# Kernel optimization log

Measured on AMD Instinct MI355X. Metric: run time of the kernel, lower is better.

## Reference

```python
import jax, jax.numpy as jnp
import numpy as np

B = 8; R = 32; BS = 4; C = 128; H = 4; MLP = 512
SHIFT = BS // 2
N = BS ** 3            # tokens per window = 64
G = R // BS            # windows per axis = 8
NW = G ** 3            # windows per sample = 512
HD = C // H


def _rel_pos_index():
    # Faithful to the torch code: only coord 0 is scaled by (3*BS-1),
    # coords 1 and 2 are just added (index collisions are intentional here).
    coords = np.stack(np.meshgrid(np.arange(BS), np.arange(BS), np.arange(BS), indexing='ij'))
    cf = coords.reshape(3, -1)
    rel = (cf[:, :, None] - cf[:, None, :]).transpose(1, 2, 0).astype(np.int64)
    rel += BS - 1
    rel[:, :, 0] *= 3 * BS - 1
    return rel.sum(-1)  # (N, N)


def _attn_mask():
    img = np.zeros((R, R, R), np.float32)
    slices = (slice(0, -BS), slice(-BS, -SHIFT), slice(-SHIFT, None))
    cnt = 0
    for sx in slices:
        for sy in slices:
            for sz in slices:
                img[sx, sy, sz] = cnt
                cnt += 1
    boxes = img.reshape(G, BS, G, BS, G, BS).transpose(0, 2, 4, 1, 3, 5).reshape(-1, N)
    d = boxes[:, None, :] - boxes[:, :, None]  # (NW, N, N)
    return np.where(d != 0, np.float32(-100.0), np.float32(0.0))


_RPI = _rel_pos_index()
_MASK = _attn_mask()


def setup_inputs() -> dict:
    key = jax.random.key(0)
    ks = jax.random.split(key, 16)
    s = 0.02
    return {
        'inputs': jax.random.normal(ks[0], (B, R ** 3, C), jnp.float32),
        'qkv_w': jax.random.normal(ks[1], (C, 3 * C), jnp.float32) * s,
        'proj_w': jax.random.normal(ks[2], (C, C), jnp.float32) * s,
        'proj_b': jnp.zeros((C,), jnp.float32),
        'bias_table': jax.random.normal(ks[3], ((3 * BS - 1) ** 2, H), jnp.float32) * s,
        'g1': jnp.ones((C,), jnp.float32),
        'b1': jnp.zeros((C,), jnp.float32),
        'g2': jnp.ones((C,), jnp.float32),
        'b2': jnp.zeros((C,), jnp.float32),
        'w1': jax.random.normal(ks[4], (C, MLP), jnp.float32) * s,
        'bb1': jnp.zeros((MLP,), jnp.float32),
        'w2': jax.random.normal(ks[5], (MLP, C), jnp.float32) * s,
        'bb2': jnp.zeros((C,), jnp.float32),
    }


def _ln(x, g, b):
    m = x.mean(-1, keepdims=True)
    v = x.var(-1, keepdims=True)
    return (x - m) * jax.lax.rsqrt(v + 1e-5) * g + b


def reference(inputs, qkv_w, proj_w, proj_b, bias_table, g1, b1, g2, b2, w1, bb1, w2, bb2):
    rpi = jnp.asarray(_RPI)
    mask = jnp.asarray(_MASK)

    x = _ln(inputs, g1, b1).reshape(B, R, R, R, C)
    x = jnp.roll(x, (-SHIFT, -SHIFT, -SHIFT), axis=(1, 2, 3))
    # box partition -> (B*NW, N, C)
    boxes = x.reshape(B, G, BS, G, BS, G, BS, C).transpose(0, 1, 3, 5, 2, 4, 6, 7).reshape(-1, N, C)

    qkv = (boxes @ qkv_w).reshape(-1, N, 3, H, HD).transpose(2, 0, 3, 1, 4)
    q, k, v = qkv[0] * (HD ** -0.5), qkv[1], qkv[2]
    attn = jnp.einsum('bhnd,bhmd->bhnm', q, k)

    bias = bias_table[rpi.reshape(-1)].reshape(N, N, H).transpose(2, 0, 1)  # (H, N, N)
    attn = attn + bias[None]
    attn = attn.reshape(B, NW, H, N, N) + mask[None, :, None]
    attn = jax.nn.softmax(attn.reshape(-1, H, N, N), axis=-1)

    out = jnp.einsum('bhnm,bhmd->bhnd', attn, v).transpose(0, 2, 1, 3).reshape(-1, N, C)
    out = out @ proj_w + proj_b

    # box reverse + unshift
    out = out.reshape(B, G, G, G, BS, BS, BS, C).transpose(0, 1, 4, 2, 5, 3, 6, 7).reshape(B, R, R, R, C)
    out = jnp.roll(out, (SHIFT, SHIFT, SHIFT), axis=(1, 2, 3)).reshape(B, R ** 3, C)

    x = out * 0.5 + inputs
    h = _ln(x, g2, b2)
    h = jax.nn.gelu(h @ w1 + bb1, approximate=False) @ w2 + bb2
    return h * 0.5 + x
```

## Files before the change

### kernel.cpp

```cpp
#include <hip/hip_runtime.h>
#include <hip/hip_bf16.h>

typedef unsigned short u16;
typedef unsigned int u32;
typedef __attribute__((ext_vector_type(8))) short short8;
typedef __attribute__((ext_vector_type(4))) float f32x4;

__device__ __forceinline__ u16 f2bf(float x) {
  __hip_bfloat16 h = __float2bfloat16(x);
  return *reinterpret_cast<u16*>(&h);
}

__global__ __launch_bounds__(256) void k_wprep4(const float* __restrict__ qkv_w,
                                                const float* __restrict__ proj_w,
                                                const float* __restrict__ w1,
                                                const float* __restrict__ w2,
                                                u16* __restrict__ qkvT, u16* __restrict__ projT,
                                                u16* __restrict__ w1T, u16* __restrict__ w2T) {
  __shared__ float tile[64][65];
  const int b = blockIdx.x, t = threadIdx.x;
  const float* src; u16* dst; int K, N, tk, tn;
  if (b < 12)      { src = qkv_w;  dst = qkvT;  K = 128; N = 384; tk = b / 6;        tn = b % 6; }
  else if (b < 16) { src = proj_w; dst = projT; K = 128; N = 128; tk = (b - 12) / 2; tn = (b - 12) % 2; }
  else if (b < 32) { src = w1;     dst = w1T;   K = 128; N = 512; tk = (b - 16) / 8; tn = (b - 16) % 8; }
  else             { src = w2;     dst = w2T;   K = 512; N = 128; tk = (b - 32) / 2; tn = (b - 32) % 2; }
  const int rb = t >> 6, c = t & 63;
  #pragma unroll
  for (int i = 0; i < 16; ++i) {
    int r = i * 4 + rb;
    tile[r][c] = src[(size_t)(tk * 64 + r) * N + tn * 64 + c];
  }
  __syncthreads();
  #pragma unroll
  for (int i = 0; i < 16; ++i) {
    int rr = i * 4 + rb;
    dst[(size_t)(tn * 64 + rr) * K + tk * 64 + c] = f2bf(tile[c][rr]);
  }
}

__global__ __launch_bounds__(256, 2) void k_all(const float* __restrict__ inputs,
                                                const u16* __restrict__ qkvT,
                                                const u16* __restrict__ projT,
                                                const float* __restrict__ proj_b,
                                                const float* __restrict__ btab,
                                                const float* __restrict__ g1,
                                                const float* __restrict__ b1,
                                                const u16* __restrict__ w1T,
                                                const u16* __restrict__ w2T,
                                                const float* __restrict__ g2,
                                                const float* __restrict__ b2,
                                                const float* __restrict__ bb1,
                                                const float* __restrict__ bb2,
                                                float* __restrict__ out) {
  __shared__ __align__(16) char lds[76800];
  u16* A_s  = (u16*)lds;
  u16* Q_s  = (u16*)(lds + 19456);
  u16* K_s  = (u16*)(lds + 36864);
  u16* P_s  = (u16*)lds;
  u16* O_s  = (u16*)(lds + 36864);
  u16* Vt_s = (u16*)(lds + 54272);
  float* bias_s = (float*)(lds + 72704);
  float* red    = (float*)(lds + 74752);
  float* X_s = (float*)lds;
  u16* A2_s  = (u16*)(lds + 36864);
  u16* H0    = (u16*)(lds + 54272);
  u16* H1    = (u16*)(lds + 63488);

  const int t = threadIdx.x, wv = t >> 6, lane = t & 63;
  const int m = lane & 15, q4 = lane >> 4;
  const int bw = blockIdx.x;
  const int wbox = bw & 511, bsm = bw >> 9;
  const int gx = wbox >> 6, gy = (wbox >> 3) & 7, gz = wbox & 7;

  for (int i = t; i < 484; i += 256) bias_s[(i & 3) * 128 + (i >> 2)] = btab[i];

  short8 bq[4][2];
  #pragma unroll
  for (int kc = 0; kc < 4; ++kc)
    #pragma unroll
    for (int nt2 = 0; nt2 < 2; ++nt2)
      bq[kc][nt2] = *(const short8*)(qkvT + (size_t)(wv * 32 + nt2 * 16 + m) * 128 + kc * 32 + q4 * 8);

  {
    const int r1 = t >> 2, seg = t & 3;
    const int ix = r1 >> 4, iy = (r1 >> 2) & 3, iz = r1 & 3;
    const int X = (gx * 4 + ix + 2) & 31, Y = (gy * 4 + iy + 2) & 31, Z = (gz * 4 + iz + 2) & 31;
    const size_t orig = ((size_t)bsm << 15) + (size_t)(X * 1024 + Y * 32 + Z);
    const float4* x4 = (const float4*)(inputs + orig * 128 + seg * 32);
    float vals[32];
    float s = 0.f, ss = 0.f;
    #pragma unroll
    for (int i = 0; i < 8; ++i) {
      float4 v = x4[i];
      vals[4 * i] = v.x; vals[4 * i + 1] = v.y; vals[4 * i + 2] = v.z; vals[4 * i + 3] = v.w;
      s += v.x + v.y + v.z + v.w;
      ss += v.x * v.x + v.y * v.y + v.z * v.z + v.w * v.w;
    }
    red[r1 * 8 + seg] = s; red[r1 * 8 + 4 + seg] = ss;
    float sum = red[r1 * 8 + 0] + red[r1 * 8 + 1] + red[r1 * 8 + 2] + red[r1 * 8 + 3];
    float sq  = red[r1 * 8 + 4] + red[r1 * 8 + 5] + red[r1 * 8 + 6] + red[r1 * 8 + 7];
    float mean = sum * 0.0078125f;
    float var = sq * 0.0078125f - mean * mean;
    float rs = rsqrtf(var + 1e-5f);
    #pragma unroll
    for (int i = 0; i < 32; ++i) {
      int c = seg * 32 + i;
      A_s[r1 * 152 + c] = f2bf((vals[i] - mean) * rs * g1[c] + b1[c]);
    }
  }
  __syncthreads();

  short8 bk[4][2];
  #pragma unroll
  for (int kc = 0; kc < 4; ++kc)
    #pragma unroll
    for (int nt2 = 0; nt2 < 2; ++nt2)
      bk[kc][nt2] = *(const short8*)(qkvT + (size_t)(128 + wv * 32 + nt2 * 16 + m) * 128 + kc * 32 + q4 * 8);

  short8 af[4][4];
  #pragma unroll
  for (int kc = 0; kc < 4; ++kc)
    #pragma unroll
    for (int mt = 0; mt < 4; ++mt)
      af[kc][mt] = *(const short8*)(A_s + (mt * 16 + m) * 152 + kc * 32 + q4 * 8);

  f32x4 zero = {0.f, 0.f, 0.f, 0.f};

  {
    f32x4 acc1[4][2];
    #pragma unroll
    for (int mt = 0; mt < 4; ++mt)
      #pragma unroll
      for (int nt2 = 0; nt2 < 2; ++nt2) acc1[mt][nt2] = zero;
    #pragma unroll
    for (int kc = 0; kc < 4; ++kc)
      #pragma unroll
      for (int mt = 0; mt < 4; ++mt)
        #pragma unroll
        for (int nt2 = 0; nt2 < 2; ++nt2)
          acc1[mt][nt2] = __builtin_amdgcn_mfma_f32_16x16x32_bf16(af[kc][mt], bq[kc][nt2], acc1[mt][nt2], 0, 0, 0);
    #pragma unroll
    for (int mt = 0; mt < 4; ++mt)
      #pragma unroll
      for (int nt2 = 0; nt2 < 2; ++nt2)
        #pragma unroll
        for (int r = 0; r < 4; ++r)
          Q_s[(mt * 16 + q4 * 4 + r) * 136 + wv * 32 + nt2 * 16 + m] =
              f2bf(acc1[mt][nt2][r] * 0.17677669529663687f);
  }

  short8 bv[4][2];
  #pragma unroll
  for (int kc = 0; kc < 4; ++kc)
    #pragma unroll
    for (int nt2 = 0; nt2 < 2; ++nt2)
      bv[kc][nt2] = *(const short8*)(qkvT + (size_t)(256 + wv * 32 + nt2 * 16 + m) * 128 + kc * 32 + q4 * 8);

  {
    f32x4 acc1[4][2];
    #pragma unroll
    for (int mt = 0; mt < 4; ++mt)
      #pragma unroll
      for (int nt2 = 0; nt2 < 2; ++nt2) acc1[mt][nt2] = zero;
    #pragma unroll
    for (int kc = 0; kc < 4; ++kc)
      #pragma unroll
      for (int mt = 0; mt < 4; ++mt)
        #pragma unroll
        for (int nt2 = 0; nt2 < 2; ++nt2)
          acc1[mt][nt2] = __builtin_amdgcn_mfma_f32_16x16x32_bf16(af[kc][mt], bk[kc][nt2], acc1[mt][nt2], 0, 0, 0);
    #pragma unroll
    for (int mt = 0; mt < 4; ++mt)
      #pragma unroll
      for (int nt2 = 0; nt2 < 2; ++nt2)
        #pragma unroll
        for (int r = 0; r < 4; ++r)
          K_s[(mt * 16 + q4 * 4 + r) * 136 + wv * 32 + nt2 * 16 + m] = f2bf(acc1[mt][nt2][r]);
  }

  {
    f32x4 acc1[4][2];
    #pragma unroll
    for (int mt = 0; mt < 4; ++mt)
      #pragma unroll
      for (int nt2 = 0; nt2 < 2; ++nt2) acc1[mt][nt2] = zero;
    #pragma unroll
    for (int kc = 0; kc < 4; ++kc)
      #pragma unroll
      for (int mt = 0; mt < 4; ++mt)
        #pragma unroll
        for (int nt2 = 0; nt2 < 2; ++nt2)
          acc1[mt][nt2] = __builtin_amdgcn_mfma_f32_16x16x32_bf16(af[kc][mt], bv[kc][nt2], acc1[mt][nt2], 0, 0, 0);
    #pragma unroll
    for (int mt = 0; mt < 4; ++mt)
      #pragma unroll
      for (int nt2 = 0; nt2 < 2; ++nt2)
        #pragma unroll
        for (int r = 0; r < 4; ++r)
          Vt_s[wv * 2304 + (nt2 * 16 + m) * 72 + mt * 16 + q4 * 4 + r] = f2bf(acc1[mt][nt2][r]);
  }

  short8 qf[4], kf[4];
  #pragma unroll
  for (int ti = 0; ti < 4; ++ti) {
    qf[ti] = *(const short8*)(Q_s + (ti * 16 + m) * 136 + wv * 32 + q4 * 8);
    kf[ti] = *(const short8*)(K_s + (ti * 16 + m) * 136 + wv * 32 + q4 * 8);
  }
  __syncthreads();

  f32x4 S[4][4];
  #pragma unroll
  for (int ti = 0; ti < 4; ++ti)
    #pragma unroll
    for (int tj = 0; tj < 4; ++tj) S[ti][tj] = zero;
  #pragma unroll
  for (int ti = 0; ti < 4; ++ti)
    #pragma unroll
    for (int tj = 0; tj < 4; ++tj)
      S[ti][tj] = __builtin_amdgcn_mfma_f32_16x16x32_bf16(qf[ti], kf[tj], S[ti][tj], 0, 0, 0);

  int catx[4], caty[4], catz[4];
  #pragma unroll
  for (int a = 0; a < 4; ++a) {
    catx[a] = (gx < 7) ? 0 : ((a < 2) ? 1 : 2);
    caty[a] = (gy < 7) ? 0 : ((a < 2) ? 1 : 2);
    catz[a] = (gz < 7) ? 0 : ((a < 2) ? 1 : 2);
  }
  const int cy = (m >> 2) & 3, cz = m & 3;
  int labc[4], labr[16];
  #pragma unroll
  for (int tj = 0; tj < 4; ++tj) labc[tj] = catx[tj] * 9 + caty[cy] * 3 + catz[cz];
  #pragma unroll
  for (int ti = 0; ti < 4; ++ti)
    #pragma unroll
    for (int r = 0; r < 4; ++r) labr[ti * 4 + r] = catx[ti] * 9 + caty[q4] * 3 + catz[r];

  #pragma unroll
  for (int ti = 0; ti < 4; ++ti)
    #pragma unroll
    for (int tj = 0; tj < 4; ++tj) {
      int K0 = 11 * (ti - tj + 3) + (q4 + 3 - cy) + (3 - cz);
      #pragma unroll
      for (int r = 0; r < 4; ++r) {
        float v = S[ti][tj][r] + bias_s[wv * 128 + K0 + r];
        if (labr[ti * 4 + r] != labc[tj]) v -= 100.f;
        S[ti][tj][r] = v;
      }
    }

  float mx[16], sm[16];
  #pragma unroll
  for (int ti = 0; ti < 4; ++ti)
    #pragma unroll
    for (int r = 0; r < 4; ++r)
      mx[ti * 4 + r] = fmaxf(fmaxf(S[ti][0][r], S[ti][1][r]), fmaxf(S[ti][2][r], S[ti][3][r]));
  #pragma unroll
  for (int off = 1; off < 16; off <<= 1)
    #pragma unroll
    for (int i = 0; i < 16; ++i) mx[i] = fmaxf(mx[i], __shfl_xor(mx[i], off, 64));
  #pragma unroll
  for (int ti = 0; ti < 4; ++ti)
    #pragma unroll
    for (int r = 0; r < 4; ++r) {
      float e0 = __expf(S[ti][0][r] - mx[ti * 4 + r]);
      float e1 = __expf(S[ti][1][r] - mx[ti * 4 + r]);
      float e2 = __expf(S[ti][2][r] - mx[ti * 4 + r]);
      float e3 = __expf(S[ti][3][r] - mx[ti * 4 + r]);
      S[ti][0][r] = e0; S[ti][1][r] = e1; S[ti][2][r] = e2; S[ti][3][r] = e3;
      sm[ti * 4 + r] = (e0 + e1) + (e2 + e3);
    }
  #pragma unroll
  for (int off = 1; off < 16; off <<= 1)
    #pragma unroll
    for (int i = 0; i < 16; ++i) sm[i] += __shfl_xor(sm[i], off, 64);
  #pragma unroll
  for (int i = 0; i < 16; ++i) sm[i] = 1.f / sm[i];

  #pragma unroll
  for (int ti = 0; ti < 4; ++ti)
    #pragma unroll
    for (int tj = 0; tj < 4; ++tj)
      #pragma unroll
      for (int r = 0; r < 4; ++r)
        P_s[wv * 4608 + (ti * 16 + q4 * 4 + r) * 72 + tj * 16 + m] = f2bf(S[ti][tj][r]);

  f32x4 O[4][2];
  #pragma unroll
  for (int ti = 0; ti < 4; ++ti)
    #pragma unroll
    for (int tv = 0; tv < 2; ++tv) O[ti][tv] = zero;
  #pragma unroll
  for (int ks = 0; ks < 2; ++ks) {
    short8 pa[4], vb[2];
    #pragma unroll
    for (int ti = 0; ti < 4; ++ti)
      pa[ti] = *(const short8*)(P_s + wv * 4608 + (ti * 16 + m) * 72 + ks * 32 + q4 * 8);
    #pragma unroll
    for (int tv = 0; tv < 2; ++tv)
      vb[tv] = *(const short8*)(Vt_s + wv * 2304 + (tv * 16 + m) * 72 + ks * 32 + q4 * 8);
    #pragma unroll
    for (int ti = 0; ti < 4; ++ti)
      #pragma unroll
      for (int tv = 0; tv < 2; ++tv)
        O[ti][tv] = __builtin_amdgcn_mfma_f32_16x16x32_bf16(pa[ti], vb[tv], O[ti][tv], 0, 0, 0);
  }

  #pragma unroll
  for (int ti = 0; ti < 4; ++ti)
    #pragma unroll
    for (int tv = 0; tv < 2; ++tv)
      #pragma unroll
      for (int r = 0; r < 4; ++r)
        O_s[(ti * 16 + q4 * 4 + r) * 136 + wv * 32 + tv * 16 + m] = f2bf(O[ti][tv][r] * sm[ti * 4 + r]);

  short8 bp[4][2];
  #pragma unroll
  for (int kc = 0; kc < 4; ++kc)
    #pragma unroll
    for (int nt2 = 0; nt2 < 2; ++nt2)
      bp[kc][nt2] = *(const short8*)(projT + (size_t)(wv * 32 + nt2 * 16 + m) * 128 + kc * 32 + q4 * 8);
  float pb[2] = {proj_b[wv * 32 + m], proj_b[wv * 32 + 16 + m]};

  __syncthreads();

  short8 af2[4][4];
  #pragma unroll
  for (int kc = 0; kc < 4; ++kc)
    #pragma unroll
    for (int mt = 0; mt < 4; ++mt)
      af2[kc][mt] = *(const short8*)(O_s + (mt * 16 + m) * 136 + kc * 32 + q4 * 8);
  f32x4 acc2[4][2];
  #pragma unroll
  for (int mt = 0; mt < 4; ++mt)
    #pragma unroll
    for (int nt2 = 0; nt2 < 2; ++nt2) acc2[mt][nt2] = zero;
  #pragma unroll
  for (int kc = 0; kc < 4; ++kc)
    #pragma unroll
    for (int mt = 0; mt < 4; ++mt)
      #pragma unroll
      for (int nt2 = 0; nt2 < 2; ++nt2)
        acc2[mt][nt2] = __builtin_amdgcn_mfma_f32_16x16x32_bf16(af2[kc][mt], bp[kc][nt2], acc2[mt][nt2], 0, 0, 0);

  #pragma unroll
  for (int mt = 0; mt < 4; ++mt)
    #pragma unroll
    for (int nt2 = 0; nt2 < 2; ++nt2)
      #pragma unroll
      for (int r = 0; r < 4; ++r)
        X_s[(mt * 16 + q4 * 4 + r) * 132 + wv * 32 + nt2 * 16 + m] = 0.5f * (acc2[mt][nt2][r] + pb[nt2]);

  __syncthreads();

  const u16* w1base = w1T + (size_t)(wv * 16 + m) * 128 + q4 * 8;
  short8 b1p0[4], b1p1[4];
  #pragma unroll
  for (int kc = 0; kc < 4; ++kc) b1p0[kc] = *(const short8*)(w1base + kc * 32);
  #pragma unroll
  for (int kc = 0; kc < 4; ++kc) b1p1[kc] = *(const short8*)(w1base + (size_t)64 * 128 + kc * 32);
  float bias1[8];
  #pragma unroll
  for (int nt = 0; nt < 8; ++nt) bias1[nt] = bb1[nt * 64 + wv * 16 + m];

  {
    const int r1 = t >> 2, seg = t & 3;
    const int ix = r1 >> 4, iy = (r1 >> 2) & 3, iz = r1 & 3;
    const int X = (gx * 4 + ix + 2) & 31, Y = (gy * 4 + iy + 2) & 31, Z = (gz * 4 + iz + 2) & 31;
    const size_t orig = ((size_t)bsm << 15) + (size_t)(X * 1024 + Y * 32 + Z);
    const float4* x4 = (const float4*)(inputs + orig * 128 + seg * 32);
    float vals[32];
    float s = 0.f, ss = 0.f;
    #pragma unroll
    for (int i = 0; i < 8; ++i) {
      float4 v = x4[i];
      float* xp = X_s + r1 * 132 + seg * 32 + 4 * i;
      float a0 = xp[0] + v.x, a1 = xp[1] + v.y, a2 = xp[2] + v.z, a3 = xp[3] + v.w;
      xp[0] = a0; xp[1] = a1; xp[2] = a2; xp[3] = a3;
      vals[4 * i] = a0; vals[4 * i + 1] = a1; vals[4 * i + 2] = a2; vals[4 * i + 3] = a3;
      s += a0 + a1 + a2 + a3;
      ss += a0 * a0 + a1 * a1 + a2 * a2 + a3 * a3;
    }
    red[r1 * 8 + seg] = s; red[r1 * 8 + 4 + seg] = ss;
    float sum = red[r1 * 8 + 0] + red[r1 * 8 + 1] + red[r1 * 8 + 2] + red[r1 * 8 + 3];
    float sq  = red[r1 * 8 + 4] + red[r1 * 8 + 5] + red[r1 * 8 + 6] + red[r1 * 8 + 7];
    float mean = sum * 0.0078125f;
    float var = sq * 0.0078125f - mean * mean;
    float rs = rsqrtf(var + 1e-5f);
    #pragma unroll
    for (int i = 0; i < 32; ++i) {
      int c = seg * 32 + i;
      A2_s[r1 * 136 + c] = f2bf((vals[i] - mean) * rs * g2[c] + b2[c]);
    }
  }
  __syncthreads();

  short8 am[4][4];
  #pragma unroll
  for (int kc = 0; kc < 4; ++kc)
    #pragma unroll
    for (int mt = 0; mt < 4; ++mt)
      am[kc][mt] = *(const short8*)(A2_s + (mt * 16 + m) * 136 + kc * 32 + q4 * 8);

  f32x4 acc[4][2];
  #pragma unroll
  for (int mt = 0; mt < 4; ++mt)
    #pragma unroll
    for (int nt2 = 0; nt2 < 2; ++nt2) acc[mt][nt2] = zero;

  #pragma unroll
  for (int nt = 0; nt < 8; ++nt) {
    u16* Hb = (nt & 1) ? H1 : H0;
    f32x4 hacc[4];
    #pragma unroll
    for (int mt = 0; mt < 4; ++mt) hacc[mt] = zero;
    if (nt & 1) {
      #pragma unroll
      for (int kc = 0; kc < 4; ++kc)
        #pragma unroll
        for (int mt = 0; mt < 4; ++mt)
          hacc[mt] = __builtin_amdgcn_mfma_f32_16x16x32_bf16(am[kc][mt], b1p1[kc], hacc[mt], 0, 0, 0);
    } else {
      #pragma unroll
      for (int kc = 0; kc < 4; ++kc)
        #pragma unroll
        for (int mt = 0; mt < 4; ++mt)
          hacc[mt] = __builtin_amdgcn_mfma_f32_16x16x32_bf16(am[kc][mt], b1p0[kc], hacc[mt], 0, 0, 0);
    }

    short8 b2f[2][2];
    #pragma unroll
    for (int kc2 = 0; kc2 < 2; ++kc2)
      #pragma unroll
      for (int nt2 = 0; nt2 < 2; ++nt2)
        b2f[kc2][nt2] = *(const short8*)(w2T + (size_t)(wv * 32 + nt2 * 16 + m) * 512 +
                                         nt * 64 + kc2 * 32 + q4 * 8);

    float bias = bias1[nt];
    #pragma unroll
    for (int mt = 0; mt < 4; ++mt)
      #pragma unroll
      for (int r = 0; r < 4; ++r) {
        float v = hacc[mt][r] + bias;
        float v2 = v * v;
        float qe = v * __builtin_fmaf(-0.07135482f, v2, -1.5957691f);
        float te = __expf(qe);
        float gl = v * __builtin_amdgcn_rcpf(1.f + te);
        Hb[(mt * 16 + q4 * 4 + r) * 72 + wv * 16 + m] = f2bf(gl);
      }
    __syncthreads();

    if (nt < 6) {
      const u16* p = w1base + (size_t)(nt + 2) * 64 * 128;
      if (nt & 1) {
        #pragma unroll
        for (int kc = 0; kc < 4; ++kc) b1p1[kc] = *(const short8*)(p + kc * 32);
      } else {
        #pragma unroll
        for (int kc = 0; kc < 4; ++kc) b1p0[kc] = *(const short8*)(p + kc * 32);
      }
    }

    #pragma unroll
    for (int kc2 = 0; kc2 < 2; ++kc2) {
      short8 a2[4];
      #pragma unroll
      for (int mt = 0; mt < 4; ++mt)
        a2[mt] = *(const short8*)(Hb + (mt * 16 + m) * 72 + kc2 * 32 + q4 * 8);
      #pragma unroll
      for (int mt = 0; mt < 4; ++mt)
        #pragma unroll
        for (int nt2 = 0; nt2 < 2; ++nt2)
          acc[mt][nt2] = __builtin_amdgcn_mfma_f32_16x16x32_bf16(a2[mt], b2f[kc2][nt2],
                                                                 acc[mt][nt2], 0, 0, 0);
    }
  }

  float ob[2] = {bb2[wv * 32 + m], bb2[wv * 32 + 16 + m]};
  #pragma unroll
  for (int mt = 0; mt < 4; ++mt)
    #pragma unroll
    for (int r = 0; r < 4; ++r) {
      int nn = mt * 16 + q4 * 4 + r;
      int ix = nn >> 4, iy = (nn >> 2) & 3, iz = nn & 3;
      int X = (gx * 4 + ix + 2) & 31, Y = (gy * 4 + iy + 2) & 31, Z = (gz * 4 + iz + 2) & 31;
      size_t orig = ((size_t)bsm << 15) + (size_t)(X * 1024 + Y * 32 + Z);
      #pragma unroll
      for (int nt2 = 0; nt2 < 2; ++nt2) {
        int col = wv * 32 + nt2 * 16 + m;
        float v = acc[mt][nt2][r] + ob[nt2];
        out[orig * 128 + col] = 0.5f * v + X_s[nn * 132 + col];
      }
    }
}

extern "C" void kernel_launch(void* const* d_in, const int* in_sizes, int n_in,
                              void* d_out, int out_size, void* d_ws, size_t ws_size,
                              hipStream_t stream) {
  const float* inputs = (const float*)d_in[0];
  const float* qkv_w  = (const float*)d_in[1];
  const float* proj_w = (const float*)d_in[2];
  const float* proj_b = (const float*)d_in[3];
  const float* btab   = (const float*)d_in[4];
  const float* g1     = (const float*)d_in[5];
  const float* b1     = (const float*)d_in[6];
  const float* g2     = (const float*)d_in[7];
  const float* b2     = (const float*)d_in[8];
  const float* w1     = (const float*)d_in[9];
  const float* bb1    = (const float*)d_in[10];
  const float* w2     = (const float*)d_in[11];
  const float* bb2    = (const float*)d_in[12];
  float* out = (float*)d_out;

  char* ws = (char*)d_ws;
  u16* qkvT  = (u16*)(ws + 0);
  u16* projT = (u16*)(ws + 98304);
  u16* w1T   = (u16*)(ws + 131072);
  u16* w2T   = (u16*)(ws + 262144);

  k_wprep4<<<48, 256, 0, stream>>>(qkv_w, proj_w, w1, w2, qkvT, projT, w1T, w2T);
  k_all<<<4096, 256, 0, stream>>>(inputs, qkvT, projT, proj_b, btab, g1, b1,
                                  w1T, w2T, g2, b2, bb1, bb2, out);
}
```

Measured before the change: 481.7 us.

## Transpose MFMA operand roles, precompute bias fragments, shrink LDS for higher occupancy

Swaps the A/B operand order in several MFMAs so accumulator rows map to tokens. This allows packed 8-byte bf16 stores to LDS and vectorised f32x4 output writes instead of scalar scatter. The relative-position bias is precomputed per lane into a global fragment buffer by an extra prep block. LayerNorm reductions now use warp shuffles instead of LDS, and the residual is kept in registers. Together these cut LDS from 75KB to 52KB and raise launch bounds to 3 blocks per CU, which risks register pressure and spills.

```diff
diff --git a/kernel.cpp b/kernel.cpp
--- a/kernel.cpp
+++ b/kernel.cpp
@@ -4,21 +4,44 @@
 typedef unsigned short u16;
 typedef unsigned int u32;
 typedef __attribute__((ext_vector_type(8))) short short8;
+typedef __attribute__((ext_vector_type(2))) unsigned int u32x2;
 typedef __attribute__((ext_vector_type(4))) float f32x4;
 
 __device__ __forceinline__ u16 f2bf(float x) {
   __hip_bfloat16 h = __float2bfloat16(x);
   return *reinterpret_cast<u16*>(&h);
 }
+__device__ __forceinline__ u32 pk2(float a, float b) {
+  return (u32)f2bf(a) | ((u32)f2bf(b) << 16);
+}
+__device__ __forceinline__ float bflo(u32 u) { return __uint_as_float(u << 16); }
+__device__ __forceinline__ float bfhi(u32 u) { return __uint_as_float(u & 0xffff0000u); }
 
 __global__ __launch_bounds__(256) void k_wprep4(const float* __restrict__ qkv_w,
                                                 const float* __restrict__ proj_w,
                                                 const float* __restrict__ w1,
                                                 const float* __restrict__ w2,
+                                                const float* __restrict__ btab,
                                                 u16* __restrict__ qkvT, u16* __restrict__ projT,
-                                                u16* __restrict__ w1T, u16* __restrict__ w2T) {
+                                                u16* __restrict__ w1T, u16* __restrict__ w2T,
+                                                u32* __restrict__ bfrag) {
+  const int b = blockIdx.x, t = threadIdx.x;
+  if (b == 48) {
+    const int h = t >> 6, m = t & 15, q4 = (t >> 4) & 3;
+    const int my = m >> 2, mz = m & 3;
+    for (int g = 0; g < 16; ++g) {
+      int ti = g >> 2, tj = g & 3;
+      int base = 11 * (tj - ti + 3) + (my - q4 + 3) + (mz + 3);
+      float v0 = btab[(base - 0) * 4 + h];
+      float v1 = btab[(base - 1) * 4 + h];
+      float v2 = btab[(base - 2) * 4 + h];
+      float v3 = btab[(base - 3) * 4 + h];
+      bfrag[(g * 256 + t) * 2 + 0] = pk2(v0, v1);
+      bfrag[(g * 256 + t) * 2 + 1] = pk2(v2, v3);
+    }
+    return;
+  }
   __shared__ float tile[64][65];
-  const int b = blockIdx.x, t = threadIdx.x;
   const float* src; u16* dst; int K, N, tk, tn;
   if (b < 12)      { src = qkv_w;  dst = qkvT;  K = 128; N = 384; tk = b / 6;        tn = b % 6; }
   else if (b < 16) { src = proj_w; dst = projT; K = 128; N = 128; tk = (b - 12) / 2; tn = (b - 12) % 2; }
@@ -38,11 +61,11 @@
   }
 }
 
-__global__ __launch_bounds__(256, 2) void k_all(const float* __restrict__ inputs,
+__global__ __launch_bounds__(256, 3) void k_all(const float* __restrict__ inputs,
                                                 const u16* __restrict__ qkvT,
                                                 const u16* __restrict__ projT,
                                                 const float* __restrict__ proj_b,
-                                                const float* __restrict__ btab,
+                                                const u32* __restrict__ bfrag,
                                                 const float* __restrict__ g1,
                                                 const float* __restrict__ b1,
                                                 const u16* __restrict__ w1T,
@@ -52,34 +75,13 @@
                                                 const float* __restrict__ bb1,
                                                 const float* __restrict__ bb2,
                                                 float* __restrict__ out) {
-  __shared__ __align__(16) char lds[76800];
-  u16* A_s  = (u16*)lds;
-  u16* Q_s  = (u16*)(lds + 19456);
-  u16* K_s  = (u16*)(lds + 36864);
-  u16* P_s  = (u16*)lds;
-  u16* O_s  = (u16*)(lds + 36864);
-  u16* Vt_s = (u16*)(lds + 54272);
-  float* bias_s = (float*)(lds + 72704);
-  float* red    = (float*)(lds + 74752);
-  float* X_s = (float*)lds;
-  u16* A2_s  = (u16*)(lds + 36864);
-  u16* H0    = (u16*)(lds + 54272);
-  u16* H1    = (u16*)(lds + 63488);
+  __shared__ __align__(16) char lds[53248];
 
   const int t = threadIdx.x, wv = t >> 6, lane = t & 63;
   const int m = lane & 15, q4 = lane >> 4;
   const int bw = blockIdx.x;
   const int wbox = bw & 511, bsm = bw >> 9;
   const int gx = wbox >> 6, gy = (wbox >> 3) & 7, gz = wbox & 7;
-
-  for (int i = t; i < 484; i += 256) bias_s[(i & 3) * 128 + (i >> 2)] = btab[i];
-
-  short8 bq[4][2];
-  #pragma unroll
-  for (int kc = 0; kc < 4; ++kc)
-    #pragma unroll
-    for (int nt2 = 0; nt2 < 2; ++nt2)
-      bq[kc][nt2] = *(const short8*)(qkvT + (size_t)(wv * 32 + nt2 * 16 + m) * 128 + kc * 32 + q4 * 8);
 
   {
     const int r1 = t >> 2, seg = t & 3;
@@ -96,116 +98,132 @@
       s += v.x + v.y + v.z + v.w;
       ss += v.x * v.x + v.y * v.y + v.z * v.z + v.w * v.w;
     }
-    red[r1 * 8 + seg] = s; red[r1 * 8 + 4 + seg] = ss;
-    float sum = red[r1 * 8 + 0] + red[r1 * 8 + 1] + red[r1 * 8 + 2] + red[r1 * 8 + 3];
-    float sq  = red[r1 * 8 + 4] + red[r1 * 8 + 5] + red[r1 * 8 + 6] + red[r1 * 8 + 7];
-    float mean = sum * 0.0078125f;
-    float var = sq * 0.0078125f - mean * mean;
+    s += __shfl_xor(s, 1, 64);  s += __shfl_xor(s, 2, 64);
+    ss += __shfl_xor(ss, 1, 64); ss += __shfl_xor(ss, 2, 64);
+    float mean = s * 0.0078125f;
+    float var = ss * 0.0078125f - mean * mean;
     float rs = rsqrtf(var + 1e-5f);
     #pragma unroll
-    for (int i = 0; i < 32; ++i) {
-      int c = seg * 32 + i;
-      A_s[r1 * 152 + c] = f2bf((vals[i] - mean) * rs * g1[c] + b1[c]);
-    }
-  }
-  __syncthreads();
-
-  short8 bk[4][2];
+    for (int v8 = 0; v8 < 4; ++v8) {
+      short8 w;
+      #pragma unroll
+      for (int j = 0; j < 8; ++j) {
+        int c = seg * 32 + v8 * 8 + j;
+        w[j] = (short)f2bf((vals[v8 * 8 + j] - mean) * rs * g1[c] + b1[c]);
+      }
+      *(short8*)(lds + r1 * 272 + seg * 64 + v8 * 16) = w;
+    }
+  }
+  __syncthreads();
+
+  short8 af[4][4];
   #pragma unroll
   for (int kc = 0; kc < 4; ++kc)
     #pragma unroll
-    for (int nt2 = 0; nt2 < 2; ++nt2)
-      bk[kc][nt2] = *(const short8*)(qkvT + (size_t)(128 + wv * 32 + nt2 * 16 + m) * 128 + kc * 32 + q4 * 8);
-
-  short8 af[4][4];
-  #pragma unroll
-  for (int kc = 0; kc < 4; ++kc)
+    for (int jt = 0; jt < 4; ++jt)
+      af[kc][jt] = *(const short8*)(lds + (jt * 16 + m) * 272 + kc * 64 + q4 * 16);
+  __syncthreads();
+
+  f32x4 zero = {0.f, 0.f, 0.f, 0.f};
+
+  {
+    short8 wq[4][2];
+    #pragma unroll
+    for (int kc = 0; kc < 4; ++kc)
+      #pragma unroll
+      for (int it = 0; it < 2; ++it)
+        wq[kc][it] = *(const short8*)(qkvT + (size_t)(wv * 32 + it * 16 + m) * 128 + kc * 32 + q4 * 8);
+    f32x4 acc[2][4];
+    #pragma unroll
+    for (int it = 0; it < 2; ++it)
+      #pragma unroll
+      for (int jt = 0; jt < 4; ++jt) acc[it][jt] = zero;
+    #pragma unroll
+    for (int kc = 0; kc < 4; ++kc)
+      #pragma unroll
+      for (int it = 0; it < 2; ++it)
+        #pragma unroll
+        for (int jt = 0; jt < 4; ++jt)
+          acc[it][jt] = __builtin_amdgcn_mfma_f32_16x16x32_bf16(wq[kc][it], af[kc][jt], acc[it][jt], 0, 0, 0);
+    #pragma unroll
+    for (int it = 0; it < 2; ++it)
+      #pragma unroll
+      for (int jt = 0; jt < 4; ++jt) {
+        f32x4 a = acc[it][jt];
+        u32x2 w = {pk2(a[0] * 0.17677669529663687f, a[1] * 0.17677669529663687f),
+                   pk2(a[2] * 0.17677669529663687f, a[3] * 0.17677669529663687f)};
+        *(u32x2*)(lds + (jt * 16 + m) * 272 + (wv * 32 + it * 16 + q4 * 4) * 2) = w;
+      }
+  }
+
+  {
+    short8 wk[4][2];
+    #pragma unroll
+    for (int kc = 0; kc < 4; ++kc)
+      #pragma unroll
+      for (int it = 0; it < 2; ++it)
+        wk[kc][it] = *(const short8*)(qkvT + (size_t)(128 + wv * 32 + it * 16 + m) * 128 + kc * 32 + q4 * 8);
+    f32x4 acc[2][4];
+    #pragma unroll
+    for (int it = 0; it < 2; ++it)
+      #pragma unroll
+      for (int jt = 0; jt < 4; ++jt) acc[it][jt] = zero;
+    #pragma unroll
+    for (int kc = 0; kc < 4; ++kc)
+      #pragma unroll
+      for (int it = 0; it < 2; ++it)
+        #pragma unroll
+        for (int jt = 0; jt < 4; ++jt)
+          acc[it][jt] = __builtin_amdgcn_mfma_f32_16x16x32_bf16(wk[kc][it], af[kc][jt], acc[it][jt], 0, 0, 0);
+    #pragma unroll
+    for (int it = 0; it < 2; ++it)
+      #pragma unroll
+      for (int jt = 0; jt < 4; ++jt) {
+        f32x4 a = acc[it][jt];
+        u32x2 w = {pk2(a[0], a[1]), pk2(a[2], a[3])};
+        *(u32x2*)(lds + 17408 + (jt * 16 + m) * 272 + (wv * 32 + it * 16 + q4 * 4) * 2) = w;
+      }
+  }
+
+  {
+    short8 wvv[4][2];
+    #pragma unroll
+    for (int kc = 0; kc < 4; ++kc)
+      #pragma unroll
+      for (int n2 = 0; n2 < 2; ++n2)
+        wvv[kc][n2] = *(const short8*)(qkvT + (size_t)(256 + wv * 32 + n2 * 16 + m) * 128 + kc * 32 + q4 * 8);
+    f32x4 acc[4][2];
     #pragma unroll
     for (int mt = 0; mt < 4; ++mt)
-      af[kc][mt] = *(const short8*)(A_s + (mt * 16 + m) * 152 + kc * 32 + q4 * 8);
-
-  f32x4 zero = {0.f, 0.f, 0.f, 0.f};
-
-  {
-    f32x4 acc1[4][2];
+      #pragma unroll
+      for (int n2 = 0; n2 < 2; ++n2) acc[mt][n2] = zero;
+    #pragma unroll
+    for (int kc = 0; kc < 4; ++kc)
+      #pragma unroll
+      for (int mt = 0; mt < 4; ++mt)
+        #pragma unroll
+        for (int n2 = 0; n2 < 2; ++n2)
+          acc[mt][n2] = __builtin_amdgcn_mfma_f32_16x16x32_bf16(af[kc][mt], wvv[kc][n2], acc[mt][n2], 0, 0, 0);
     #pragma unroll
     for (int mt = 0; mt < 4; ++mt)
       #pragma unroll
-      for (int nt2 = 0; nt2 < 2; ++nt2) acc1[mt][nt2] = zero;
-    #pragma unroll
-    for (int kc = 0; kc < 4; ++kc)
-      #pragma unroll
-      for (int mt = 0; mt < 4; ++mt)
-        #pragma unroll
-        for (int nt2 = 0; nt2 < 2; ++nt2)
-          acc1[mt][nt2] = __builtin_amdgcn_mfma_f32_16x16x32_bf16(af[kc][mt], bq[kc][nt2], acc1[mt][nt2], 0, 0, 0);
-    #pragma unroll
-    for (int mt = 0; mt < 4; ++mt)
-      #pragma unroll
-      for (int nt2 = 0; nt2 < 2; ++nt2)
-        #pragma unroll
-        for (int r = 0; r < 4; ++r)
-          Q_s[(mt * 16 + q4 * 4 + r) * 136 + wv * 32 + nt2 * 16 + m] =
-              f2bf(acc1[mt][nt2][r] * 0.17677669529663687f);
-  }
-
-  short8 bv[4][2];
-  #pragma unroll
-  for (int kc = 0; kc < 4; ++kc)
-    #pragma unroll
-    for (int nt2 = 0; nt2 < 2; ++nt2)
-      bv[kc][nt2] = *(const short8*)(qkvT + (size_t)(256 + wv * 32 + nt2 * 16 + m) * 128 + kc * 32 + q4 * 8);
-
-  {
-    f32x4 acc1[4][2];
-    #pragma unroll
-    for (int mt = 0; mt < 4; ++mt)
-      #pragma unroll
-      for (int nt2 = 0; nt2 < 2; ++nt2) acc1[mt][nt2] = zero;
-    #pragma unroll
-    for (int kc = 0; kc < 4; ++kc)
-      #pragma unroll
-      for (int mt = 0; mt < 4; ++mt)
-        #pragma unroll
-        for (int nt2 = 0; nt2 < 2; ++nt2)
-          acc1[mt][nt2] = __builtin_amdgcn_mfma_f32_16x16x32_bf16(af[kc][mt], bk[kc][nt2], acc1[mt][nt2], 0, 0, 0);
-    #pragma unroll
-    for (int mt = 0; mt < 4; ++mt)
-      #pragma unroll
-      for (int nt2 = 0; nt2 < 2; ++nt2)
-        #pragma unroll
-        for (int r = 0; r < 4; ++r)
-          K_s[(mt * 16 + q4 * 4 + r) * 136 + wv * 32 + nt2 * 16 + m] = f2bf(acc1[mt][nt2][r]);
-  }
-
-  {
-    f32x4 acc1[4][2];
-    #pragma unroll
-    for (int mt = 0; mt < 4; ++mt)
-      #pragma unroll
-      for (int nt2 = 0; nt2 < 2; ++nt2) acc1[mt][nt2] = zero;
-    #pragma unroll
-    for (int kc = 0; kc < 4; ++kc)
-      #pragma unroll
-      for (int mt = 0; mt < 4; ++mt)
-        #pragma unroll
-        for (int nt2 = 0; nt2 < 2; ++nt2)
-          acc1[mt][nt2] = __builtin_amdgcn_mfma_f32_16x16x32_bf16(af[kc][mt], bv[kc][nt2], acc1[mt][nt2], 0, 0, 0);
-    #pragma unroll
-    for (int mt = 0; mt < 4; ++mt)
-      #pragma unroll
-      for (int nt2 = 0; nt2 < 2; ++nt2)
-        #pragma unroll
-        for (int r = 0; r < 4; ++r)
-          Vt_s[wv * 2304 + (nt2 * 16 + m) * 72 + mt * 16 + q4 * 4 + r] = f2bf(acc1[mt][nt2][r]);
+      for (int n2 = 0; n2 < 2; ++n2) {
+        f32x4 a = acc[mt][n2];
+        u32x2 w = {pk2(a[0], a[1]), pk2(a[2], a[3])};
+        *(u32x2*)(lds + 34816 + wv * 4608 + (n2 * 16 + m) * 144 + mt * 32 + q4 * 8) = w;
+      }
   }
 
   short8 qf[4], kf[4];
   #pragma unroll
   for (int ti = 0; ti < 4; ++ti) {
-    qf[ti] = *(const short8*)(Q_s + (ti * 16 + m) * 136 + wv * 32 + q4 * 8);
-    kf[ti] = *(const short8*)(K_s + (ti * 16 + m) * 136 + wv * 32 + q4 * 8);
-  }
+    qf[ti] = *(const short8*)(lds + (ti * 16 + m) * 272 + wv * 64 + q4 * 16);
+    kf[ti] = *(const short8*)(lds + 17408 + (ti * 16 + m) * 272 + wv * 64 + q4 * 16);
+  }
+  u32x2 bu[16];
+  #pragma unroll
+  for (int g = 0; g < 16; ++g)
+    bu[g] = *(const u32x2*)(bfrag + (g * 256 + t) * 2);
   __syncthreads();
 
   f32x4 S[4][4];
@@ -217,7 +235,7 @@
   for (int ti = 0; ti < 4; ++ti)
     #pragma unroll
     for (int tj = 0; tj < 4; ++tj)
-      S[ti][tj] = __builtin_amdgcn_mfma_f32_16x16x32_bf16(qf[ti], kf[tj], S[ti][tj], 0, 0, 0);
+      S[ti][tj] = __builtin_amdgcn_mfma_f32_16x16x32_bf16(kf[ti], qf[tj], S[ti][tj], 0, 0, 0);
 
   int catx[4], caty[4], catz[4];
   #pragma unroll
@@ -227,130 +245,215 @@
     catz[a] = (gz < 7) ? 0 : ((a < 2) ? 1 : 2);
   }
   const int cy = (m >> 2) & 3, cz = m & 3;
-  int labc[4], labr[16];
-  #pragma unroll
-  for (int tj = 0; tj < 4; ++tj) labc[tj] = catx[tj] * 9 + caty[cy] * 3 + catz[cz];
+  int labq[4], labk[16];
+  #pragma unroll
+  for (int tj = 0; tj < 4; ++tj) labq[tj] = catx[tj] * 9 + caty[cy] * 3 + catz[cz];
   #pragma unroll
   for (int ti = 0; ti < 4; ++ti)
     #pragma unroll
-    for (int r = 0; r < 4; ++r) labr[ti * 4 + r] = catx[ti] * 9 + caty[q4] * 3 + catz[r];
+    for (int rr = 0; rr < 4; ++rr) labk[ti * 4 + rr] = catx[ti] * 9 + caty[q4] * 3 + catz[rr];
 
   #pragma unroll
   for (int ti = 0; ti < 4; ++ti)
     #pragma unroll
     for (int tj = 0; tj < 4; ++tj) {
-      int K0 = 11 * (ti - tj + 3) + (q4 + 3 - cy) + (3 - cz);
-      #pragma unroll
-      for (int r = 0; r < 4; ++r) {
-        float v = S[ti][tj][r] + bias_s[wv * 128 + K0 + r];
-        if (labr[ti * 4 + r] != labc[tj]) v -= 100.f;
-        S[ti][tj][r] = v;
-      }
-    }
-
-  float mx[16], sm[16];
+      u32x2 bp = bu[ti * 4 + tj];
+      #pragma unroll
+      for (int rr = 0; rr < 4; ++rr) {
+        float bv = (rr & 1) ? bfhi(bp[rr >> 1]) : bflo(bp[rr >> 1]);
+        float v = S[ti][tj][rr] + bv;
+        if (labk[ti * 4 + rr] != labq[tj]) v -= 100.f;
+        S[ti][tj][rr] = v;
+      }
+    }
+
+  float mx[4], sm[4];
+  #pragma unroll
+  for (int tj = 0; tj < 4; ++tj) {
+    float v = fmaxf(fmaxf(S[0][tj][0], S[0][tj][1]), fmaxf(S[0][tj][2], S[0][tj][3]));
+    #pragma unroll
+    for (int ti = 1; ti < 4; ++ti)
+      v = fmaxf(v, fmaxf(fmaxf(S[ti][tj][0], S[ti][tj][1]), fmaxf(S[ti][tj][2], S[ti][tj][3])));
+    v = fmaxf(v, __shfl_xor(v, 16, 64));
+    v = fmaxf(v, __shfl_xor(v, 32, 64));
+    mx[tj] = v;
+  }
+  #pragma unroll
+  for (int tj = 0; tj < 4; ++tj) {
+    float s = 0.f;
+    #pragma unroll
+    for (int ti = 0; ti < 4; ++ti)
+      #pragma unroll
+      for (int rr = 0; rr < 4; ++rr) {
+        float e = __expf(S[ti][tj][rr] - mx[tj]);
+        S[ti][tj][rr] = e;
+        s += e;
+      }
+    s += __shfl_xor(s, 16, 64);
+    s += __shfl_xor(s, 32, 64);
+    sm[tj] = 1.f / s;
+  }
+
   #pragma unroll
   for (int ti = 0; ti < 4; ++ti)
     #pragma unroll
-    for (int r = 0; r < 4; ++r)
-      mx[ti * 4 + r] = fmaxf(fmaxf(S[ti][0][r], S[ti][1][r]), fmaxf(S[ti][2][r], S[ti][3][r]));
-  #pragma unroll
-  for (int off = 1; off < 16; off <<= 1)
-    #pragma unroll
-    for (int i = 0; i < 16; ++i) mx[i] = fmaxf(mx[i], __shfl_xor(mx[i], off, 64));
-  #pragma unroll
-  for (int ti = 0; ti < 4; ++ti)
-    #pragma unroll
-    for (int r = 0; r < 4; ++r) {
-      float e0 = __expf(S[ti][0][r] - mx[ti * 4 + r]);
-      float e1 = __expf(S[ti][1][r] - mx[ti * 4 + r]);
-      float e2 = __expf(S[ti][2][r] - mx[ti * 4 + r]);
-      float e3 = __expf(S[ti][3][r] - mx[ti * 4 + r]);
-      S[ti][0][r] = e0; S[ti][1][r] = e1; S[ti][2][r] = e2; S[ti][3][r] = e3;
-      sm[ti * 4 + r] = (e0 + e1) + (e2 + e3);
-    }
-  #pragma unroll
-  for (int off = 1; off < 16; off <<= 1)
-    #pragma unroll
-    for (int i = 0; i < 16; ++i) sm[i] += __shfl_xor(sm[i], off, 64);
-  #pragma unroll
-  for (int i = 0; i < 16; ++i) sm[i] = 1.f / sm[i];
-
-  #pragma unroll
-  for (int ti = 0; ti < 4; ++ti)
-    #pragma unroll
-    for (int tj = 0; tj < 4; ++tj)
-      #pragma unroll
-      for (int r = 0; r < 4; ++r)
-        P_s[wv * 4608 + (ti * 16 + q4 * 4 + r) * 72 + tj * 16 + m] = f2bf(S[ti][tj][r]);
-
-  f32x4 O[4][2];
-  #pragma unroll
-  for (int ti = 0; ti < 4; ++ti)
-    #pragma unroll
-    for (int tv = 0; tv < 2; ++tv) O[ti][tv] = zero;
+    for (int tj = 0; tj < 4; ++tj) {
+      f32x4 a = S[ti][tj];
+      u32x2 w = {pk2(a[0], a[1]), pk2(a[2], a[3])};
+      *(u32x2*)(lds + wv * 8704 + (tj * 16 + m) * 136 + ti * 32 + q4 * 8) = w;
+    }
+
+  f32x4 accO[2][4];
+  #pragma unroll
+  for (int it = 0; it < 2; ++it)
+    #pragma unroll
+    for (int jt = 0; jt < 4; ++jt) accO[it][jt] = zero;
   #pragma unroll
   for (int ks = 0; ks < 2; ++ks) {
-    short8 pa[4], vb[2];
-    #pragma unroll
-    for (int ti = 0; ti < 4; ++ti)
-      pa[ti] = *(const short8*)(P_s + wv * 4608 + (ti * 16 + m) * 72 + ks * 32 + q4 * 8);
-    #pragma unroll
-    for (int tv = 0; tv < 2; ++tv)
-      vb[tv] = *(const short8*)(Vt_s + wv * 2304 + (tv * 16 + m) * 72 + ks * 32 + q4 * 8);
-    #pragma unroll
-    for (int ti = 0; ti < 4; ++ti)
-      #pragma unroll
-      for (int tv = 0; tv < 2; ++tv)
-        O[ti][tv] = __builtin_amdgcn_mfma_f32_16x16x32_bf16(pa[ti], vb[tv], O[ti][tv], 0, 0, 0);
-  }
-
-  #pragma unroll
-  for (int ti = 0; ti < 4; ++ti)
-    #pragma unroll
-    for (int tv = 0; tv < 2; ++tv)
-      #pragma unroll
-      for (int r = 0; r < 4; ++r)
-        O_s[(ti * 16 + q4 * 4 + r) * 136 + wv * 32 + tv * 16 + m] = f2bf(O[ti][tv][r] * sm[ti * 4 + r]);
-
-  short8 bp[4][2];
+    short8 vb[2], pa[4];
+    #pragma unroll
+    for (int it = 0; it < 2; ++it)
+      vb[it] = *(const short8*)(lds + 34816 + wv * 4608 + (it * 16 + m) * 144 + ks * 64 + q4 * 16);
+    #pragma unroll
+    for (int jt = 0; jt < 4; ++jt) {
+      u32x2 lo = *(const u32x2*)(lds + wv * 8704 + (jt * 16 + m) * 136 + ks * 64 + q4 * 16);
+      u32x2 hi = *(const u32x2*)(lds + wv * 8704 + (jt * 16 + m) * 136 + ks * 64 + q4 * 16 + 8);
+      union { u32 u[4]; short8 s; } c;
+      c.u[0] = lo[0]; c.u[1] = lo[1]; c.u[2] = hi[0]; c.u[3] = hi[1];
+      pa[jt] = c.s;
+    }
+    #pragma unroll
+    for (int it = 0; it < 2; ++it)
+      #pragma unroll
+      for (int jt = 0; jt < 4; ++jt)
+        accO[it][jt] = __builtin_amdgcn_mfma_f32_16x16x32_bf16(vb[it], pa[jt], accO[it][jt], 0, 0, 0);
+  }
+  __syncthreads();
+
+  #pragma unroll
+  for (int it = 0; it < 2; ++it)
+    #pragma unroll
+    for (int jt = 0; jt < 4; ++jt) {
+      f32x4 a = accO[it][jt];
+      float sc = sm[jt];
+      u32x2 w = {pk2(a[0] * sc, a[1] * sc), pk2(a[2] * sc, a[3] * sc)};
+      *(u32x2*)(lds + (jt * 16 + m) * 272 + (wv * 32 + it * 16 + q4 * 4) * 2) = w;
+    }
+  __syncthreads();
+
+  int origjt[4];
+  #pragma unroll
+  for (int jt = 0; jt < 4; ++jt) {
+    int X = (gx * 4 + jt + 2) & 31, Y = (gy * 4 + (m >> 2) + 2) & 31, Z = (gz * 4 + (m & 3) + 2) & 31;
+    origjt[jt] = (bsm << 15) + X * 1024 + Y * 32 + Z;
+  }
+  f32x4 xr[2][4];
+  {
+    short8 bp[4][2], of[4][4];
+    #pragma unroll
+    for (int kc = 0; kc < 4; ++kc)
+      #pragma unroll
+      for (int it = 0; it < 2; ++it)
+        bp[kc][it] = *(const short8*)(projT + (size_t)(wv * 32 + it * 16 + m) * 128 + kc * 32 + q4 * 8);
+    f32x4 inr[2][4];
+    #pragma unroll
+    for (int it = 0; it < 2; ++it)
+      #pragma unroll
+      for (int jt = 0; jt < 4; ++jt)
+        inr[it][jt] = *(const f32x4*)(inputs + (size_t)origjt[jt] * 128 + wv * 32 + it * 16 + q4 * 4);
+    f32x4 pbv[2];
+    #pragma unroll
+    for (int it = 0; it < 2; ++it)
+      pbv[it] = *(const f32x4*)(proj_b + wv * 32 + it * 16 + q4 * 4);
+    #pragma unroll
+    for (int kc = 0; kc < 4; ++kc)
+      #pragma unroll
+      for (int jt = 0; jt < 4; ++jt)
+        of[kc][jt] = *(const short8*)(lds + (jt * 16 + m) * 272 + kc * 64 + q4 * 16);
+    f32x4 acc[2][4];
+    #pragma unroll
+    for (int it = 0; it < 2; ++it)
+      #pragma unroll
+      for (int jt = 0; jt < 4; ++jt) acc[it][jt] = zero;
+    #pragma unroll
+    for (int kc = 0; kc < 4; ++kc)
+      #pragma unroll
+      for (int it = 0; it < 2; ++it)
+        #pragma unroll
+        for (int jt = 0; jt < 4; ++jt)
+          acc[it][jt] = __builtin_amdgcn_mfma_f32_16x16x32_bf16(bp[kc][it], of[kc][jt], acc[it][jt], 0, 0, 0);
+    #pragma unroll
+    for (int it = 0; it < 2; ++it)
+      #pragma unroll
+      for (int jt = 0; jt < 4; ++jt)
+        #pragma unroll
+        for (int rr = 0; rr < 4; ++rr)
+          xr[it][jt][rr] = 0.5f * (acc[it][jt][rr] + pbv[it][rr]) + inr[it][jt][rr];
+  }
+  __syncthreads();
+
+  float* red = (float*)(lds + 34816);
+  {
+    float sp[4], ssp[4];
+    #pragma unroll
+    for (int jt = 0; jt < 4; ++jt) {
+      float s = 0.f, ss2 = 0.f;
+      #pragma unroll
+      for (int it = 0; it < 2; ++it)
+        #pragma unroll
+        for (int rr = 0; rr < 4; ++rr) {
+          float v = xr[it][jt][rr];
+          s += v; ss2 += v * v;
+        }
+      s += __shfl_xor(s, 16, 64);  s += __shfl_xor(s, 32, 64);
+      ss2 += __shfl_xor(ss2, 16, 64); ss2 += __shfl_xor(ss2, 32, 64);
+      sp[jt] = s; ssp[jt] = ss2;
+    }
+    if (q4 == 0) {
+      #pragma unroll
+      for (int jt = 0; jt < 4; ++jt) {
+        red[(jt * 16 + m) * 8 + wv * 2 + 0] = sp[jt];
+        red[(jt * 16 + m) * 8 + wv * 2 + 1] = ssp[jt];
+      }
+    }
+  }
+  __syncthreads();
+
+  {
+    f32x4 g2v[2], b2v[2];
+    #pragma unroll
+    for (int it = 0; it < 2; ++it) {
+      g2v[it] = *(const f32x4*)(g2 + wv * 32 + it * 16 + q4 * 4);
+      b2v[it] = *(const f32x4*)(b2 + wv * 32 + it * 16 + q4 * 4);
+    }
+    #pragma unroll
+    for (int jt = 0; jt < 4; ++jt) {
+      f32x4 r0 = *(const f32x4*)(red + (jt * 16 + m) * 8);
+      f32x4 r1 = *(const f32x4*)(red + (jt * 16 + m) * 8 + 4);
+      float sum = r0[0] + r0[2] + r1[0] + r1[2];
+      float sq  = r0[1] + r0[3] + r1[1] + r1[3];
+      float mean = sum * 0.0078125f;
+      float var = sq * 0.0078125f - mean * mean;
+      float rs = rsqrtf(var + 1e-5f);
+      #pragma unroll
+      for (int it = 0; it < 2; ++it) {
+        float n0 = (xr[it][jt][0] - mean) * rs * g2v[it][0] + b2v[it][0];
+        float n1 = (xr[it][jt][1] - mean) * rs * g2v[it][1] + b2v[it][1];
+        float n2 = (xr[it][jt][2] - mean) * rs * g2v[it][2] + b2v[it][2];
+        float n3 = (xr[it][jt][3] - mean) * rs * g2v[it][3] + b2v[it][3];
+        u32x2 w = {pk2(n0, n1), pk2(n2, n3)};
+        *(u32x2*)(lds + 17408 + (jt * 16 + m) * 272 + (wv * 32 + it * 16 + q4 * 4) * 2) = w;
+      }
+    }
+  }
+  __syncthreads();
+
+  short8 am[4][4];
   #pragma unroll
   for (int kc = 0; kc < 4; ++kc)
     #pragma unroll
-    for (int nt2 = 0; nt2 < 2; ++nt2)
-      bp[kc][nt2] = *(const short8*)(projT + (size_t)(wv * 32 + nt2 * 16 + m) * 128 + kc * 32 + q4 * 8);
-  float pb[2] = {proj_b[wv * 32 + m], proj_b[wv * 32 + 16 + m]};
-
-  __syncthreads();
-
-  short8 af2[4][4];
-  #pragma unroll
-  for (int kc = 0; kc < 4; ++kc)
-    #pragma unroll
-    for (int mt = 0; mt < 4; ++mt)
-      af2[kc][mt] = *(const short8*)(O_s + (mt * 16 + m) * 136 + kc * 32 + q4 * 8);
-  f32x4 acc2[4][2];
-  #pragma unroll
-  for (int mt = 0; mt < 4; ++mt)
-    #pragma unroll
-    for (int nt2 = 0; nt2 < 2; ++nt2) acc2[mt][nt2] = zero;
-  #pragma unroll
-  for (int kc = 0; kc < 4; ++kc)
-    #pragma unroll
-    for (int mt = 0; mt < 4; ++mt)
-      #pragma unroll
-      for (int nt2 = 0; nt2 < 2; ++nt2)
-        acc2[mt][nt2] = __builtin_amdgcn_mfma_f32_16x16x32_bf16(af2[kc][mt], bp[kc][nt2], acc2[mt][nt2], 0, 0, 0);
-
-  #pragma unroll
-  for (int mt = 0; mt < 4; ++mt)
-    #pragma unroll
-    for (int nt2 = 0; nt2 < 2; ++nt2)
-      #pragma unroll
-      for (int r = 0; r < 4; ++r)
-        X_s[(mt * 16 + q4 * 4 + r) * 132 + wv * 32 + nt2 * 16 + m] = 0.5f * (acc2[mt][nt2][r] + pb[nt2]);
-
-  __syncthreads();
+    for (int jt = 0; jt < 4; ++jt)
+      am[kc][jt] = *(const short8*)(lds + 17408 + (jt * 16 + m) * 272 + kc * 64 + q4 * 16);
 
   const u16* w1base = w1T + (size_t)(wv * 16 + m) * 128 + q4 * 8;
   short8 b1p0[4], b1p1[4];
@@ -358,95 +461,54 @@
   for (int kc = 0; kc < 4; ++kc) b1p0[kc] = *(const short8*)(w1base + kc * 32);
   #pragma unroll
   for (int kc = 0; kc < 4; ++kc) b1p1[kc] = *(const short8*)(w1base + (size_t)64 * 128 + kc * 32);
-  float bias1[8];
-  #pragma unroll
-  for (int nt = 0; nt < 8; ++nt) bias1[nt] = bb1[nt * 64 + wv * 16 + m];
-
-  {
-    const int r1 = t >> 2, seg = t & 3;
-    const int ix = r1 >> 4, iy = (r1 >> 2) & 3, iz = r1 & 3;
-    const int X = (gx * 4 + ix + 2) & 31, Y = (gy * 4 + iy + 2) & 31, Z = (gz * 4 + iz + 2) & 31;
-    const size_t orig = ((size_t)bsm << 15) + (size_t)(X * 1024 + Y * 32 + Z);
-    const float4* x4 = (const float4*)(inputs + orig * 128 + seg * 32);
-    float vals[32];
-    float s = 0.f, ss = 0.f;
-    #pragma unroll
-    for (int i = 0; i < 8; ++i) {
-      float4 v = x4[i];
-      float* xp = X_s + r1 * 132 + seg * 32 + 4 * i;
-      float a0 = xp[0] + v.x, a1 = xp[1] + v.y, a2 = xp[2] + v.z, a3 = xp[3] + v.w;
-      xp[0] = a0; xp[1] = a1; xp[2] = a2; xp[3] = a3;
-      vals[4 * i] = a0; vals[4 * i + 1] = a1; vals[4 * i + 2] = a2; vals[4 * i + 3] = a3;
-      s += a0 + a1 + a2 + a3;
-      ss += a0 * a0 + a1 * a1 + a2 * a2 + a3 * a3;
-    }
-    red[r1 * 8 + seg] = s; red[r1 * 8 + 4 + seg] = ss;
-    float sum = red[r1 * 8 + 0] + red[r1 * 8 + 1] + red[r1 * 8 + 2] + red[r1 * 8 + 3];
-    float sq  = red[r1 * 8 + 4] + red[r1 * 8 + 5] + red[r1 * 8 + 6] + red[r1 * 8 + 7];
-    float mean = sum * 0.0078125f;
-    float var = sq * 0.0078125f - mean * mean;
-    float rs = rsqrtf(var + 1e-5f);
-    #pragma unroll
-    for (int i = 0; i < 32; ++i) {
-      int c = seg * 32 + i;
-      A2_s[r1 * 136 + c] = f2bf((vals[i] - mean) * rs * g2[c] + b2[c]);
-    }
-  }
-  __syncthreads();
-
-  short8 am[4][4];
-  #pragma unroll
-  for (int kc = 0; kc < 4; ++kc)
-    #pragma unroll
-    for (int mt = 0; mt < 4; ++mt)
-      am[kc][mt] = *(const short8*)(A2_s + (mt * 16 + m) * 136 + kc * 32 + q4 * 8);
-
-  f32x4 acc[4][2];
-  #pragma unroll
-  for (int mt = 0; mt < 4; ++mt)
-    #pragma unroll
-    for (int nt2 = 0; nt2 < 2; ++nt2) acc[mt][nt2] = zero;
+
+  f32x4 acc[2][4];
+  #pragma unroll
+  for (int it = 0; it < 2; ++it)
+    #pragma unroll
+    for (int jt = 0; jt < 4; ++jt) acc[it][jt] = zero;
 
   #pragma unroll
   for (int nt = 0; nt < 8; ++nt) {
-    u16* Hb = (nt & 1) ? H1 : H0;
+    char* Hb = lds + 34816 + (nt & 1) * 9216;
     f32x4 hacc[4];
     #pragma unroll
-    for (int mt = 0; mt < 4; ++mt) hacc[mt] = zero;
+    for (int jt = 0; jt < 4; ++jt) hacc[jt] = zero;
     if (nt & 1) {
       #pragma unroll
       for (int kc = 0; kc < 4; ++kc)
         #pragma unroll
-        for (int mt = 0; mt < 4; ++mt)
-          hacc[mt] = __builtin_amdgcn_mfma_f32_16x16x32_bf16(am[kc][mt], b1p1[kc], hacc[mt], 0, 0, 0);
+        for (int jt = 0; jt < 4; ++jt)
+          hacc[jt] = __builtin_amdgcn_mfma_f32_16x16x32_bf16(b1p1[kc], am[kc][jt], hacc[jt], 0, 0, 0);
     } else {
       #pragma unroll
       for (int kc = 0; kc < 4; ++kc)
         #pragma unroll
-        for (int mt = 0; mt < 4; ++mt)
-          hacc[mt] = __builtin_amdgcn_mfma_f32_16x16x32_bf16(am[kc][mt], b1p0[kc], hacc[mt], 0, 0, 0);
-    }
-
-    short8 b2f[2][2];
+        for (int jt = 0; jt < 4; ++jt)
+          hacc[jt] = __builtin_amdgcn_mfma_f32_16x16x32_bf16(b1p0[kc], am[kc][jt], hacc[jt], 0, 0, 0);
+    }
+    short8 a2w[2][2];
     #pragma unroll
     for (int kc2 = 0; kc2 < 2; ++kc2)
       #pragma unroll
-      for (int nt2 = 0; nt2 < 2; ++nt2)
-        b2f[kc2][nt2] = *(const short8*)(w2T + (size_t)(wv * 32 + nt2 * 16 + m) * 512 +
-                                         nt * 64 + kc2 * 32 + q4 * 8);
-
-    float bias = bias1[nt];
-    #pragma unroll
-    for (int mt = 0; mt < 4; ++mt)
-      #pragma unroll
-      for (int r = 0; r < 4; ++r) {
-        float v = hacc[mt][r] + bias;
+      for (int it = 0; it < 2; ++it)
+        a2w[kc2][it] = *(const short8*)(w2T + (size_t)(wv * 32 + it * 16 + m) * 512 +
+                                       nt * 64 + kc2 * 32 + q4 * 8);
+    f32x4 b1v = *(const f32x4*)(bb1 + nt * 64 + wv * 16 + q4 * 4);
+    #pragma unroll
+    for (int jt = 0; jt < 4; ++jt) {
+      float g[4];
+      #pragma unroll
+      for (int rr = 0; rr < 4; ++rr) {
+        float v = hacc[jt][rr] + b1v[rr];
         float v2 = v * v;
         float qe = v * __builtin_fmaf(-0.07135482f, v2, -1.5957691f);
         float te = __expf(qe);
-        float gl = v * __builtin_amdgcn_rcpf(1.f + te);
-        Hb[(mt * 16 + q4 * 4 + r) * 72 + wv * 16 + m] = f2bf(gl);
-      }
+        g[rr] = v * __builtin_amdgcn_rcpf(1.f + te);
+      }
+      u32x2 w = {pk2(g[0], g[1]), pk2(g[2], g[3])};
+      *(u32x2*)(Hb + (jt * 16 + m) * 144 + wv * 32 + q4 * 8) = w;
+    }
     __syncthreads();
 
     if (nt < 6) {
@@ -462,34 +524,31 @@
 
     #pragma unroll
     for (int kc2 = 0; kc2 < 2; ++kc2) {
-      short8 a2[4];
-      #pragma unroll
-      for (int mt = 0; mt < 4; ++mt)
-        a2[mt] = *(const short8*)(Hb + (mt * 16 + m) * 72 + kc2 * 32 + q4 * 8);
-      #pragma unroll
-      for (int mt = 0; mt < 4; ++mt)
-        #pragma unroll
-        for (int nt2 = 0; nt2 < 2; ++nt2)
-          acc[mt][nt2] = __builtin_amdgcn_mfma_f32_16x16x32_bf16(a2[mt], b2f[kc2][nt2],
-                                                                 acc[mt][nt2], 0, 0, 0);
-    }
-  }
-
-  float ob[2] = {bb2[wv * 32 + m], bb2[wv * 32 + 16 + m]};
-  #pragma unroll
-  for (int mt = 0; mt < 4; ++mt)
-    #pragma unroll
-    for (int r = 0; r < 4; ++r) {
-      int nn = mt * 16 + q4 * 4 + r;
-      int ix = nn >> 4, iy = (nn >> 2) & 3, iz = nn & 3;
-      int X = (gx * 4 + ix + 2) & 31, Y = (gy * 4 + iy + 2) & 31, Z = (gz * 4 + iz + 2) & 31;
-      size_t orig = ((size_t)bsm << 15) + (size_t)(X * 1024 + Y * 32 + Z);
-      #pragma unroll
-      for (int nt2 = 0; nt2 < 2; ++nt2) {
-        int col = wv * 32 + nt2 * 16 + m;
-        float v = acc[mt][nt2][r] + ob[nt2];
-        out[orig * 128 + col] = 0.5f * v + X_s[nn * 132 + col];
-      }
+      short8 hf[4];
+      #pragma unroll
+      for (int jt = 0; jt < 4; ++jt)
+        hf[jt] = *(const short8*)(Hb + (jt * 16 + m) * 144 + kc2 * 64 + q4 * 16);
+      #pragma unroll
+      for (int it = 0; it < 2; ++it)
+        #pragma unroll
+        for (int jt = 0; jt < 4; ++jt)
+          acc[it][jt] = __builtin_amdgcn_mfma_f32_16x16x32_bf16(a2w[kc2][it], hf[jt], acc[it][jt], 0, 0, 0);
+    }
+  }
+
+  f32x4 ob[2];
+  #pragma unroll
+  for (int it = 0; it < 2; ++it)
+    ob[it] = *(const f32x4*)(bb2 + wv * 32 + it * 16 + q4 * 4);
+  #pragma unroll
+  for (int it = 0; it < 2; ++it)
+    #pragma unroll
+    for (int jt = 0; jt < 4; ++jt) {
+      f32x4 v;
+      #pragma unroll
+      for (int rr = 0; rr < 4; ++rr)
+        v[rr] = 0.5f * (acc[it][jt][rr] + ob[it][rr]) + xr[it][jt][rr];
+      *(f32x4*)(out + (size_t)origjt[jt] * 128 + wv * 32 + it * 16 + q4 * 4) = v;
     }
 }
 
@@ -516,8 +575,9 @@
   u16* projT = (u16*)(ws + 98304);
   u16* w1T   = (u16*)(ws + 131072);
   u16* w2T   = (u16*)(ws + 262144);
-
-  k_wprep4<<<48, 256, 0, stream>>>(qkv_w, proj_w, w1, w2, qkvT, projT, w1T, w2T);
-  k_all<<<4096, 256, 0, stream>>>(inputs, qkvT, projT, proj_b, btab, g1, b1,
+  u32* bfrag = (u32*)(ws + 393216);
+
+  k_wprep4<<<49, 256, 0, stream>>>(qkv_w, proj_w, w1, w2, btab, qkvT, projT, w1T, w2T, bfrag);
+  k_all<<<4096, 256, 0, stream>>>(inputs, qkvT, projT, proj_b, bfrag, g1, b1,
                                   w1T, w2T, g2, b2, bb1, bb2, out);
 }
```

Result: slower. 512.8 us (+6.5%).
